# Optimization experiments

Measured on AMD Instinct MI355X. Metric: run time of the kernel, lower is better.

Reference implementation:

```python
import jax, jax.numpy as jnp
import numpy as np

N = 100000      # nodes
E = 1600000     # edges (avg degree 16)
D_IN = 64
D_OUT = 64
EPS = 1e-9


def setup_inputs() -> dict:
    key = jax.random.key(0)
    ks = jax.random.split(key, 12)
    x = jax.random.normal(ks[0], (N, D_IN), dtype=jnp.float32)
    edge_row = jax.random.randint(ks[1], (E,), 0, N, dtype=jnp.int32)
    edge_col = jax.random.randint(ks[2], (E,), 0, N, dtype=jnp.int32)
    # positive normalized adjacency values (~1/degree scale)
    edge_val = jax.random.uniform(ks[3], (E,), dtype=jnp.float32) / 16.0
    lim = float(np.sqrt(6.0 / (D_IN + D_OUT)))  # xavier_uniform
    W0 = jax.random.uniform(ks[4], (D_OUT, D_IN), jnp.float32, -lim, lim)
    W1 = jax.random.uniform(ks[5], (D_OUT, D_IN), jnp.float32, -lim, lim)
    b0 = jnp.zeros((D_OUT,), jnp.float32)
    b1 = jnp.zeros((D_OUT,), jnp.float32)
    scale0 = jnp.ones((D_OUT,), jnp.float32)
    scale1 = jnp.ones((D_OUT,), jnp.float32)
    offset0 = jnp.zeros((D_OUT,), jnp.float32)
    offset1 = jnp.zeros((D_OUT,), jnp.float32)
    return {"x": x, "edge_val": edge_val, "W0": W0, "b0": b0,
            "scale0": scale0, "offset0": offset0, "W1": W1, "b1": b1,
            "scale1": scale1, "offset1": offset1,
            "edge_row": edge_row, "edge_col": edge_col}


def _hop_transform(feat, W, b, scale, offset):
    # Linear (no bias in nn.Linear) + separate bias + ReLU
    h = jax.nn.relu(feat @ W.T + b)                      # [N, D_OUT]
    # custom per-row normalization ('norm' branch)
    mean = jnp.mean(h, axis=1, keepdims=True)
    var = jnp.var(h, axis=1, keepdims=True) + EPS        # unbiased=False
    return (h - mean) * scale * jax.lax.rsqrt(var) + offset


def reference(x, edge_val, W0, b0, scale0, offset0, W1, b1, scale1, offset1,
              edge_row, edge_col):
    # SpMM: out[r] = sum_{e: row[e]==r} val[e] * x[col[e]]
    msgs = edge_val[:, None] * x[edge_col]               # [E, D_IN]
    agg = jax.ops.segment_sum(msgs, edge_row, num_segments=N)
    # order=1: hop-0 uses raw features, hop-1 uses aggregated features
    h0 = _hop_transform(x, W0, b0, scale0, offset0)
    h1 = _hop_transform(agg, W1, b1, scale1, offset1)
    # aggr='mean' -> elementwise sum of partial features
    return h0 + h1
```

## Files before the change

### kernel.cpp

```cpp
#include <hip/hip_runtime.h>

#define NN 100000
#define NE 1600000
#define DD 64
#define NB   391
#define BCAP 4608
#define SCAP 6656
#define GCAP 2400000
#define NK3  1563

__device__ __forceinline__ unsigned short f2bfu(float f) {
    union { float f; unsigned u; } c; c.f = f;
    unsigned lsb = (c.u >> 16) & 1u;
    c.u += 0x7FFFu + lsb;
    return (unsigned short)(c.u >> 16);
}

typedef short v8s __attribute__((ext_vector_type(8)));
typedef float v4f __attribute__((ext_vector_type(4)));

__global__ __launch_bounds__(256) void init_kernel(
    const float* __restrict__ W0, const float* __restrict__ W1,
    int* __restrict__ gbcur, int* __restrict__ gtail,
    unsigned short* __restrict__ wb0, unsigned short* __restrict__ wb1)
{
    int i = blockIdx.x * 256 + threadIdx.x;
    if (i < NB) gbcur[i] = 0;
    if (i == 0) *gtail = 0;
    if (i < DD * DD) { wb0[i] = f2bfu(W0[i]); wb1[i] = f2bfu(W1[i]); }
}

__global__ __launch_bounds__(256) void x2bf_kernel(
    const float* __restrict__ x, unsigned short* __restrict__ xb)
{
    int i = (blockIdx.x * 256 + threadIdx.x) * 8;
    float4 a = *(const float4*)(x + i);
    float4 b = *(const float4*)(x + i + 4);
    uint4 o;
    o.x = (unsigned)f2bfu(a.x) | ((unsigned)f2bfu(a.y) << 16);
    o.y = (unsigned)f2bfu(a.z) | ((unsigned)f2bfu(a.w) << 16);
    o.z = (unsigned)f2bfu(b.x) | ((unsigned)f2bfu(b.y) << 16);
    o.w = (unsigned)f2bfu(b.z) | ((unsigned)f2bfu(b.w) << 16);
    *(uint4*)(xb + i) = o;
}

__global__ __launch_bounds__(512) void bin_scatter_kernel(
    const int* __restrict__ row, const int* __restrict__ col,
    const float* __restrict__ val, int* __restrict__ gbcur,
    int2* __restrict__ bslab)
{
    __shared__ int2 rbuf[4096];
    __shared__ unsigned short bkts[4096];
    __shared__ int pscan[512];
    __shared__ int cnt[NB];
    __shared__ int pst[NB];
    __shared__ int cur[NB];
    __shared__ int gbase[NB];

    int b = blockIdx.x, t = threadIdx.x;
    int e0 = b * 4096;

    for (int i = t; i < NB; i += 512) cnt[i] = 0;
    __syncthreads();

    int4 r[2], c[2]; float4 v[2]; bool ok[2];
#pragma unroll
    for (int h = 0; h < 2; ++h) {
        int e = e0 + t * 8 + h * 4;
        ok[h] = (e + 3 < NE);
        if (ok[h]) {
            r[h] = *(const int4*)(row + e);
            c[h] = *(const int4*)(col + e);
            v[h] = *(const float4*)(val + e);
            atomicAdd(&cnt[r[h].x >> 8], 1);
            atomicAdd(&cnt[r[h].y >> 8], 1);
            atomicAdd(&cnt[r[h].z >> 8], 1);
            atomicAdd(&cnt[r[h].w >> 8], 1);
        }
    }
    __syncthreads();
    pscan[t] = (t < NB) ? cnt[t] : 0;
    __syncthreads();
    for (int off = 1; off < 512; off <<= 1) {
        int u = (t >= off) ? pscan[t - off] : 0;
        __syncthreads();
        pscan[t] += u;
        __syncthreads();
    }
    if (t < NB) {
        int st = pscan[t] - cnt[t];
        pst[t] = st;
        cur[t] = st;
        gbase[t] = cnt[t] ? atomicAdd(&gbcur[t], cnt[t]) : 0;
    }
    __syncthreads();
#pragma unroll
    for (int h = 0; h < 2; ++h) {
        if (ok[h]) {
            int bk, pos;
            bk = r[h].x >> 8; pos = atomicAdd(&cur[bk], 1);
            rbuf[pos] = make_int2(c[h].x | ((r[h].x & 255) << 17), __float_as_int(v[h].x));
            bkts[pos] = (unsigned short)bk;
            bk = r[h].y >> 8; pos = atomicAdd(&cur[bk], 1);
            rbuf[pos] = make_int2(c[h].y | ((r[h].y & 255) << 17), __float_as_int(v[h].y));
            bkts[pos] = (unsigned short)bk;
            bk = r[h].z >> 8; pos = atomicAdd(&cur[bk], 1);
            rbuf[pos] = make_int2(c[h].z | ((r[h].z & 255) << 17), __float_as_int(v[h].z));
            bkts[pos] = (unsigned short)bk;
            bk = r[h].w >> 8; pos = atomicAdd(&cur[bk], 1);
            rbuf[pos] = make_int2(c[h].w | ((r[h].w & 255) << 17), __float_as_int(v[h].w));
            bkts[pos] = (unsigned short)bk;
        }
    }
    __syncthreads();
    int ntot = pscan[511];
    for (int i = t; i < ntot; i += 512) {
        int bk = bkts[i];
        int gi = gbase[bk] + (i - pst[bk]);
        if (gi < BCAP) bslab[(size_t)bk * BCAP + gi] = rbuf[i];
    }
}

__global__ __launch_bounds__(512) void row_sort_kernel(
    const int* __restrict__ gbcur, const int2* __restrict__ bslab,
    int* __restrict__ gtail, int2* __restrict__ gsorted,
    int* __restrict__ meta)
{
    __shared__ int2 sorted[SCAP];
    __shared__ int cnt[256];
    __shared__ int pscan[256];
    __shared__ int rcur[256];
    __shared__ int pstart[257];
    __shared__ int sh_base8;

    int b = blockIdx.x, t = threadIdx.x;
    int nb = min(gbcur[b], BCAP);
    const int2* bp = bslab + (size_t)b * BCAP;

    int2 rec[9]; int rl[9]; int nr = 0;
    if (t < 256) cnt[t] = 0;
    __syncthreads();
#pragma unroll
    for (int k = 0; k < 9; ++k) {
        int i = t + k * 512;
        if (i < nb) {
            rec[nr] = bp[i];
            rl[nr] = (rec[nr].x >> 17) & 255;
            atomicAdd(&cnt[rl[nr]], 1);
            ++nr;
        }
    }
    __syncthreads();
    if (t < 256) pscan[t] = (cnt[t] + 7) & ~7;
    __syncthreads();
    for (int off = 1; off < 256; off <<= 1) {
        int u = 0;
        if (t < 256 && t >= off) u = pscan[t - off];
        __syncthreads();
        if (t < 256) pscan[t] += u;
        __syncthreads();
    }
    if (t < 256) pstart[t + 1] = pscan[t];
    if (t == 0) {
        pstart[0] = 0;
        sh_base8 = atomicAdd(gtail, pscan[255] >> 3);
    }
    __syncthreads();
    int base8 = sh_base8;
    if (t < 256) {
        rcur[t] = pstart[t];
        int s = pstart[t] + cnt[t], e = pstart[t + 1];
        for (int j = s; j < e; ++j) sorted[j] = make_int2(0, 0);
        int n = b * 256 + t;
        int cc = min((e - pstart[t]) >> 3, 16);
        int s8 = base8 + (pstart[t] >> 3);
        meta[n] = (s8 << 5) | cc;
    }
    __syncthreads();
#pragma unroll
    for (int k = 0; k < 9; ++k) {
        if (k < nr) {
            int pos = atomicAdd(&rcur[rl[k]], 1);
            if (pos < SCAP) sorted[pos] = make_int2(rec[k].x & 0x1FFFF, rec[k].y);
        }
    }
    __syncthreads();
    int tp = pscan[255];
    int gb = base8 * 8;
    for (int i = t; i < tp; i += 512) {
        int gi = gb + i;
        if (gi < GCAP) gsorted[gi] = sorted[i];
    }
}

#define BF4FMA(G, VV, ACC) { \
    ACC.x = fmaf(VV, __uint_as_float((G).x << 16), ACC.x); \
    ACC.y = fmaf(VV, __uint_as_float((G).x & 0xFFFF0000u), ACC.y); \
    ACC.z = fmaf(VV, __uint_as_float((G).y << 16), ACC.z); \
    ACC.w = fmaf(VV, __uint_as_float((G).y & 0xFFFF0000u), ACC.w); }

__global__ __launch_bounds__(256, 8) void pull_mfma_kernel(
    const unsigned short* __restrict__ xb, const int* __restrict__ meta,
    const int2* __restrict__ gsorted,
    const unsigned short* __restrict__ wb0, const unsigned short* __restrict__ wb1,
    const float* __restrict__ b0, const float* __restrict__ s0, const float* __restrict__ o0,
    const float* __restrict__ b1, const float* __restrict__ s1, const float* __restrict__ o1,
    float* __restrict__ out)
{
    __shared__ int2 ebuf[4][128];
    __shared__ unsigned aggt[4][16][36];

    int t = threadIdx.x, lane = t & 63, wv = t >> 6;
    int sub = lane & 15, q = lane >> 4;
    int nb0 = blockIdx.x * 64 + wv * 16;
    if (nb0 >= NN) return;

    for (int rr = 0; rr < 16; ++rr) {
        int mt = meta[nb0 + rr];
        int cc = mt & 31;
        const int2* rp = gsorted + ((size_t)(mt >> 5) << 3);
        int plen = cc * 8;
        if (lane < plen) ebuf[wv][lane] = rp[lane];
        if (64 + lane < plen) ebuf[wv][64 + lane] = rp[64 + lane];

        float4 acc = make_float4(0.f, 0.f, 0.f, 0.f);
        int ch = 0;
        for (; ch + 2 <= cc; ch += 2) {
            int2 r0 = ebuf[wv][ch * 8 + q];
            int2 r1 = ebuf[wv][ch * 8 + 4 + q];
            int2 r2 = ebuf[wv][ch * 8 + 8 + q];
            int2 r3 = ebuf[wv][ch * 8 + 12 + q];
            uint2 g0 = *(const uint2*)(xb + (size_t)r0.x * DD + sub * 4);
            uint2 g1 = *(const uint2*)(xb + (size_t)r1.x * DD + sub * 4);
            uint2 g2 = *(const uint2*)(xb + (size_t)r2.x * DD + sub * 4);
            uint2 g3 = *(const uint2*)(xb + (size_t)r3.x * DD + sub * 4);
            float v0 = __int_as_float(r0.y), v1 = __int_as_float(r1.y);
            float v2 = __int_as_float(r2.y), v3 = __int_as_float(r3.y);
            BF4FMA(g0, v0, acc); BF4FMA(g1, v1, acc);
            BF4FMA(g2, v2, acc); BF4FMA(g3, v3, acc);
        }
        if (ch < cc) {
            int2 r0 = ebuf[wv][ch * 8 + q];
            int2 r1 = ebuf[wv][ch * 8 + 4 + q];
            uint2 g0 = *(const uint2*)(xb + (size_t)r0.x * DD + sub * 4);
            uint2 g1 = *(const uint2*)(xb + (size_t)r1.x * DD + sub * 4);
            float v0 = __int_as_float(r0.y), v1 = __int_as_float(r1.y);
            BF4FMA(g0, v0, acc); BF4FMA(g1, v1, acc);
        }
        acc.x += __shfl_xor(acc.x, 16, 64); acc.y += __shfl_xor(acc.y, 16, 64);
        acc.z += __shfl_xor(acc.z, 16, 64); acc.w += __shfl_xor(acc.w, 16, 64);
        acc.x += __shfl_xor(acc.x, 32, 64); acc.y += __shfl_xor(acc.y, 32, 64);
        acc.z += __shfl_xor(acc.z, 32, 64); acc.w += __shfl_xor(acc.w, 32, 64);
        if (q == 0) {
            uint2 pk;
            pk.x = (unsigned)f2bfu(acc.x) | ((unsigned)f2bfu(acc.y) << 16);
            pk.y = (unsigned)f2bfu(acc.z) | ((unsigned)f2bfu(acc.w) << 16);
            *(uint2*)&aggt[wv][rr][sub * 2] = pk;
        }
    }

    v8s ax[2], aa[2];
#pragma unroll
    for (int ks = 0; ks < 2; ++ks) {
        ax[ks] = *(const v8s*)(xb + (size_t)(nb0 + sub) * DD + ks * 32 + q * 8);
        aa[ks] = *(const v8s*)&aggt[wv][sub][ks * 16 + q * 4];
    }

    float h0v[4][4], h1v[4][4];
    float sr0[4] = {0,0,0,0}, sq0[4] = {0,0,0,0};
    float sr1[4] = {0,0,0,0}, sq1[4] = {0,0,0,0};
#pragma unroll
    for (int dt = 0; dt < 4; ++dt) {
        int nidx = dt * 16 + sub;
        float bi0 = b0[nidx], bi1 = b1[nidx];
        v8s w00 = *(const v8s*)(wb0 + nidx * 64 + q * 8);
        v8s w01 = *(const v8s*)(wb0 + nidx * 64 + 32 + q * 8);
        v8s w10 = *(const v8s*)(wb1 + nidx * 64 + q * 8);
        v8s w11 = *(const v8s*)(wb1 + nidx * 64 + 32 + q * 8);
        v4f c0 = (v4f){bi0, bi0, bi0, bi0};
        v4f c1 = (v4f){bi1, bi1, bi1, bi1};
        c0 = __builtin_amdgcn_mfma_f32_16x16x32_bf16(ax[0], w00, c0, 0, 0, 0);
        c0 = __builtin_amdgcn_mfma_f32_16x16x32_bf16(ax[1], w01, c0, 0, 0, 0);
        c1 = __builtin_amdgcn_mfma_f32_16x16x32_bf16(aa[0], w10, c1, 0, 0, 0);
        c1 = __builtin_amdgcn_mfma_f32_16x16x32_bf16(aa[1], w11, c1, 0, 0, 0);
#pragma unroll
        for (int r = 0; r < 4; ++r) {
            float h = fmaxf(c0[r], 0.f); h0v[dt][r] = h; sr0[r] += h; sq0[r] += h * h;
            float g = fmaxf(c1[r], 0.f); h1v[dt][r] = g; sr1[r] += g; sq1[r] += g * g;
        }
    }
#pragma unroll
    for (int off = 1; off < 16; off <<= 1) {
#pragma unroll
        for (int r = 0; r < 4; ++r) {
            sr0[r] += __shfl_xor(sr0[r], off, 64);
            sq0[r] += __shfl_xor(sq0[r], off, 64);
            sr1[r] += __shfl_xor(sr1[r], off, 64);
            sq1[r] += __shfl_xor(sq1[r], off, 64);
        }
    }

    float scl0[4], scl1[4], ofs0[4], ofs1[4];
#pragma unroll
    for (int dt = 0; dt < 4; ++dt) {
        int nidx = dt * 16 + sub;
        scl0[dt] = s0[nidx]; scl1[dt] = s1[nidx];
        ofs0[dt] = o0[nidx]; ofs1[dt] = o1[nidx];
    }

    const float inv = 1.0f / 64.0f;
#pragma unroll
    for (int r = 0; r < 4; ++r) {
        float m0 = sr0[r] * inv;
        float v0 = fmaxf(sq0[r] * inv - m0 * m0, 0.f) + 1e-9f;
        float m1 = sr1[r] * inv;
        float v1 = fmaxf(sq1[r] * inv - m1 * m1, 0.f) + 1e-9f;
        float rs0 = rsqrtf(v0), rs1 = rsqrtf(v1);
        int node = nb0 + q * 4 + r;
#pragma unroll
        for (int dt = 0; dt < 4; ++dt) {
            float rv = (h0v[dt][r] - m0) * scl0[dt] * rs0 + ofs0[dt]
                     + (h1v[dt][r] - m1) * scl1[dt] * rs1 + ofs1[dt];
            out[(size_t)node * DD + dt * 16 + sub] = rv;
        }
    }
}

extern "C" void kernel_launch(void* const* d_in, const int* in_sizes, int n_in,
                              void* d_out, int out_size, void* d_ws, size_t ws_size,
                              hipStream_t stream) {
    const float* x  = (const float*)d_in[0];
    const float* ev = (const float*)d_in[1];
    const float* W0 = (const float*)d_in[2];
    const float* b0 = (const float*)d_in[3];
    const float* s0 = (const float*)d_in[4];
    const float* o0 = (const float*)d_in[5];
    const float* W1 = (const float*)d_in[6];
    const float* b1 = (const float*)d_in[7];
    const float* s1 = (const float*)d_in[8];
    const float* o1 = (const float*)d_in[9];
    const int* row = (const int*)d_in[10];
    const int* col = (const int*)d_in[11];

    char* wsb = (char*)d_ws;
    int*  gbcur = (int*)wsb;
    int*  gtail = (int*)(wsb + 1600);
    unsigned short* wb0 = (unsigned short*)(wsb + 1664);
    unsigned short* wb1 = (unsigned short*)(wsb + 9856);
    int*  meta  = (int*)(wsb + 18176);
    unsigned short* xb = (unsigned short*)(wsb + 418816);
    int2* bslab = (int2*)(wsb + 13218816);
    int2* gsorted = (int2*)(wsb + 27632640);

    init_kernel<<<16, 256, 0, stream>>>(W0, W1, gbcur, gtail, wb0, wb1);
    x2bf_kernel<<<3125, 256, 0, stream>>>(x, xb);
    bin_scatter_kernel<<<NB, 512, 0, stream>>>(row, col, ev, gbcur, bslab);
    row_sort_kernel<<<NB, 512, 0, stream>>>(gbcur, bslab, gtail, gsorted, meta);
    pull_mfma_kernel<<<NK3, 256, 0, stream>>>(
        xb, meta, gsorted, wb0, wb1, b0, s0, o0, b1, s1, o1, (float*)d_out);
}
```

Baseline: 193.3 us.

## Fuse per-row sort into the pull kernel and drop the row_sort pass

Removes the separate row-sort kernel and its global sorted edge buffer. Each pull block now rescans its 256-row bucket slab, keeps only the edges for its 64-row quarter, and builds per-row edge lists in shared memory. The bin-scatter kernel handles 2048 edges per block, doubling the grid, and pull blocks are remapped in an XCD-aware way so the four quarters of a bucket share L2. The trade-off is that every bucket slab is read four times, occupancy is lower (launch bounds 5, larger LDS), and per-row degree is capped at 40 edges, so higher-degree rows would silently drop edges.

```diff
diff --git a/kernel.cpp b/kernel.cpp
--- a/kernel.cpp
+++ b/kernel.cpp
@@ -4,9 +4,9 @@
 #define NE 1600000
 #define DD 64
 #define NB   391
+#define NBK1 782
 #define BCAP 4608
-#define SCAP 6656
-#define GCAP 2400000
+#define RCAP 40
 #define NK3  1563
 
 __device__ __forceinline__ unsigned short f2bfu(float f) {
@@ -21,12 +21,11 @@
 
 __global__ __launch_bounds__(256) void init_kernel(
     const float* __restrict__ W0, const float* __restrict__ W1,
-    int* __restrict__ gbcur, int* __restrict__ gtail,
+    int* __restrict__ gbcur,
     unsigned short* __restrict__ wb0, unsigned short* __restrict__ wb1)
 {
     int i = blockIdx.x * 256 + threadIdx.x;
     if (i < NB) gbcur[i] = 0;
-    if (i == 0) *gtail = 0;
     if (i < DD * DD) { wb0[i] = f2bfu(W0[i]); wb1[i] = f2bfu(W1[i]); }
 }
 
@@ -49,8 +48,8 @@
     const float* __restrict__ val, int* __restrict__ gbcur,
     int2* __restrict__ bslab)
 {
-    __shared__ int2 rbuf[4096];
-    __shared__ unsigned short bkts[4096];
+    __shared__ int2 rbuf[2048];
+    __shared__ unsigned short bkts[2048];
     __shared__ int pscan[512];
     __shared__ int cnt[NB];
     __shared__ int pst[NB];
@@ -58,25 +57,21 @@
     __shared__ int gbase[NB];
 
     int b = blockIdx.x, t = threadIdx.x;
-    int e0 = b * 4096;
+    int e = b * 2048 + t * 4;
+    bool ok = (e + 3 < NE);
 
     for (int i = t; i < NB; i += 512) cnt[i] = 0;
     __syncthreads();
 
-    int4 r[2], c[2]; float4 v[2]; bool ok[2];
-#pragma unroll
-    for (int h = 0; h < 2; ++h) {
-        int e = e0 + t * 8 + h * 4;
-        ok[h] = (e + 3 < NE);
-        if (ok[h]) {
-            r[h] = *(const int4*)(row + e);
-            c[h] = *(const int4*)(col + e);
-            v[h] = *(const float4*)(val + e);
-            atomicAdd(&cnt[r[h].x >> 8], 1);
-            atomicAdd(&cnt[r[h].y >> 8], 1);
-            atomicAdd(&cnt[r[h].z >> 8], 1);
-            atomicAdd(&cnt[r[h].w >> 8], 1);
-        }
+    int4 r, c; float4 v;
+    if (ok) {
+        r = *(const int4*)(row + e);
+        c = *(const int4*)(col + e);
+        v = *(const float4*)(val + e);
+        atomicAdd(&cnt[r.x >> 8], 1);
+        atomicAdd(&cnt[r.y >> 8], 1);
+        atomicAdd(&cnt[r.z >> 8], 1);
+        atomicAdd(&cnt[r.w >> 8], 1);
     }
     __syncthreads();
     pscan[t] = (t < NB) ? cnt[t] : 0;
@@ -94,23 +89,20 @@
         gbase[t] = cnt[t] ? atomicAdd(&gbcur[t], cnt[t]) : 0;
     }
     __syncthreads();
-#pragma unroll
-    for (int h = 0; h < 2; ++h) {
-        if (ok[h]) {
-            int bk, pos;
-            bk = r[h].x >> 8; pos = atomicAdd(&cur[bk], 1);
-            rbuf[pos] = make_int2(c[h].x | ((r[h].x & 255) << 17), __float_as_int(v[h].x));
-            bkts[pos] = (unsigned short)bk;
-            bk = r[h].y >> 8; pos = atomicAdd(&cur[bk], 1);
-            rbuf[pos] = make_int2(c[h].y | ((r[h].y & 255) << 17), __float_as_int(v[h].y));
-            bkts[pos] = (unsigned short)bk;
-            bk = r[h].z >> 8; pos = atomicAdd(&cur[bk], 1);
-            rbuf[pos] = make_int2(c[h].z | ((r[h].z & 255) << 17), __float_as_int(v[h].z));
-            bkts[pos] = (unsigned short)bk;
-            bk = r[h].w >> 8; pos = atomicAdd(&cur[bk], 1);
-            rbuf[pos] = make_int2(c[h].w | ((r[h].w & 255) << 17), __float_as_int(v[h].w));
-            bkts[pos] = (unsigned short)bk;
-        }
+    if (ok) {
+        int bk, pos;
+        bk = r.x >> 8; pos = atomicAdd(&cur[bk], 1);
+        rbuf[pos] = make_int2(c.x | ((r.x & 255) << 17), __float_as_int(v.x));
+        bkts[pos] = (unsigned short)bk;
+        bk = r.y >> 8; pos = atomicAdd(&cur[bk], 1);
+        rbuf[pos] = make_int2(c.y | ((r.y & 255) << 17), __float_as_int(v.y));
+        bkts[pos] = (unsigned short)bk;
+        bk = r.z >> 8; pos = atomicAdd(&cur[bk], 1);
+        rbuf[pos] = make_int2(c.z | ((r.z & 255) << 17), __float_as_int(v.z));
+        bkts[pos] = (unsigned short)bk;
+        bk = r.w >> 8; pos = atomicAdd(&cur[bk], 1);
+        rbuf[pos] = make_int2(c.w | ((r.w & 255) << 17), __float_as_int(v.w));
+        bkts[pos] = (unsigned short)bk;
     }
     __syncthreads();
     int ntot = pscan[511];
@@ -121,207 +113,155 @@
     }
 }
 
-__global__ __launch_bounds__(512) void row_sort_kernel(
-    const int* __restrict__ gbcur, const int2* __restrict__ bslab,
-    int* __restrict__ gtail, int2* __restrict__ gsorted,
-    int* __restrict__ meta)
-{
-    __shared__ int2 sorted[SCAP];
-    __shared__ int cnt[256];
-    __shared__ int pscan[256];
-    __shared__ int rcur[256];
-    __shared__ int pstart[257];
-    __shared__ int sh_base8;
-
-    int b = blockIdx.x, t = threadIdx.x;
-    int nb = min(gbcur[b], BCAP);
-    const int2* bp = bslab + (size_t)b * BCAP;
-
-    int2 rec[9]; int rl[9]; int nr = 0;
-    if (t < 256) cnt[t] = 0;
-    __syncthreads();
-#pragma unroll
-    for (int k = 0; k < 9; ++k) {
-        int i = t + k * 512;
-        if (i < nb) {
-            rec[nr] = bp[i];
-            rl[nr] = (rec[nr].x >> 17) & 255;
-            atomicAdd(&cnt[rl[nr]], 1);
-            ++nr;
-        }
-    }
-    __syncthreads();
-    if (t < 256) pscan[t] = (cnt[t] + 7) & ~7;
-    __syncthreads();
-    for (int off = 1; off < 256; off <<= 1) {
-        int u = 0;
-        if (t < 256 && t >= off) u = pscan[t - off];
-        __syncthreads();
-        if (t < 256) pscan[t] += u;
-        __syncthreads();
-    }
-    if (t < 256) pstart[t + 1] = pscan[t];
-    if (t == 0) {
-        pstart[0] = 0;
-        sh_base8 = atomicAdd(gtail, pscan[255] >> 3);
-    }
-    __syncthreads();
-    int base8 = sh_base8;
-    if (t < 256) {
-        rcur[t] = pstart[t];
-        int s = pstart[t] + cnt[t], e = pstart[t + 1];
-        for (int j = s; j < e; ++j) sorted[j] = make_int2(0, 0);
-        int n = b * 256 + t;
-        int cc = min((e - pstart[t]) >> 3, 16);
-        int s8 = base8 + (pstart[t] >> 3);
-        meta[n] = (s8 << 5) | cc;
-    }
-    __syncthreads();
-#pragma unroll
-    for (int k = 0; k < 9; ++k) {
-        if (k < nr) {
-            int pos = atomicAdd(&rcur[rl[k]], 1);
-            if (pos < SCAP) sorted[pos] = make_int2(rec[k].x & 0x1FFFF, rec[k].y);
-        }
-    }
-    __syncthreads();
-    int tp = pscan[255];
-    int gb = base8 * 8;
-    for (int i = t; i < tp; i += 512) {
-        int gi = gb + i;
-        if (gi < GCAP) gsorted[gi] = sorted[i];
-    }
-}
-
 #define BF4FMA(G, VV, ACC) { \
     ACC.x = fmaf(VV, __uint_as_float((G).x << 16), ACC.x); \
     ACC.y = fmaf(VV, __uint_as_float((G).x & 0xFFFF0000u), ACC.y); \
     ACC.z = fmaf(VV, __uint_as_float((G).y << 16), ACC.z); \
     ACC.w = fmaf(VV, __uint_as_float((G).y & 0xFFFF0000u), ACC.w); }
 
-__global__ __launch_bounds__(256, 8) void pull_mfma_kernel(
-    const unsigned short* __restrict__ xb, const int* __restrict__ meta,
-    const int2* __restrict__ gsorted,
+__global__ __launch_bounds__(256, 5) void sort_pull_mfma_kernel(
+    const unsigned short* __restrict__ xb, const int* __restrict__ gbcur,
+    const int2* __restrict__ bslab,
     const unsigned short* __restrict__ wb0, const unsigned short* __restrict__ wb1,
     const float* __restrict__ b0, const float* __restrict__ s0, const float* __restrict__ o0,
     const float* __restrict__ b1, const float* __restrict__ s1, const float* __restrict__ o1,
     float* __restrict__ out)
 {
-    __shared__ int2 ebuf[4][128];
+    __shared__ int2 ebuf[64][RCAP];
     __shared__ unsigned aggt[4][16][36];
+    __shared__ int cur[64];
+
+    int phys = blockIdx.x;
+    int xc = phys & 7, ii = phys >> 3;
+    int p = (xc < 3) ? xc * 196 + ii : 588 + (xc - 3) * 195 + ii;
 
     int t = threadIdx.x, lane = t & 63, wv = t >> 6;
     int sub = lane & 15, q = lane >> 4;
-    int nb0 = blockIdx.x * 64 + wv * 16;
-    if (nb0 >= NN) return;
-
-    for (int rr = 0; rr < 16; ++rr) {
-        int mt = meta[nb0 + rr];
-        int cc = mt & 31;
-        const int2* rp = gsorted + ((size_t)(mt >> 5) << 3);
-        int plen = cc * 8;
-        if (lane < plen) ebuf[wv][lane] = rp[lane];
-        if (64 + lane < plen) ebuf[wv][64 + lane] = rp[64 + lane];
-
-        float4 acc = make_float4(0.f, 0.f, 0.f, 0.f);
-        int ch = 0;
-        for (; ch + 2 <= cc; ch += 2) {
-            int2 r0 = ebuf[wv][ch * 8 + q];
-            int2 r1 = ebuf[wv][ch * 8 + 4 + q];
-            int2 r2 = ebuf[wv][ch * 8 + 8 + q];
-            int2 r3 = ebuf[wv][ch * 8 + 12 + q];
-            uint2 g0 = *(const uint2*)(xb + (size_t)r0.x * DD + sub * 4);
-            uint2 g1 = *(const uint2*)(xb + (size_t)r1.x * DD + sub * 4);
-            uint2 g2 = *(const uint2*)(xb + (size_t)r2.x * DD + sub * 4);
-            uint2 g3 = *(const uint2*)(xb + (size_t)r3.x * DD + sub * 4);
-            float v0 = __int_as_float(r0.y), v1 = __int_as_float(r1.y);
-            float v2 = __int_as_float(r2.y), v3 = __int_as_float(r3.y);
-            BF4FMA(g0, v0, acc); BF4FMA(g1, v1, acc);
-            BF4FMA(g2, v2, acc); BF4FMA(g3, v3, acc);
-        }
-        if (ch < cc) {
-            int2 r0 = ebuf[wv][ch * 8 + q];
-            int2 r1 = ebuf[wv][ch * 8 + 4 + q];
-            uint2 g0 = *(const uint2*)(xb + (size_t)r0.x * DD + sub * 4);
-            uint2 g1 = *(const uint2*)(xb + (size_t)r1.x * DD + sub * 4);
-            float v0 = __int_as_float(r0.y), v1 = __int_as_float(r1.y);
-            BF4FMA(g0, v0, acc); BF4FMA(g1, v1, acc);
-        }
-        acc.x += __shfl_xor(acc.x, 16, 64); acc.y += __shfl_xor(acc.y, 16, 64);
-        acc.z += __shfl_xor(acc.z, 16, 64); acc.w += __shfl_xor(acc.w, 16, 64);
-        acc.x += __shfl_xor(acc.x, 32, 64); acc.y += __shfl_xor(acc.y, 32, 64);
-        acc.z += __shfl_xor(acc.z, 32, 64); acc.w += __shfl_xor(acc.w, 32, 64);
-        if (q == 0) {
-            uint2 pk;
-            pk.x = (unsigned)f2bfu(acc.x) | ((unsigned)f2bfu(acc.y) << 16);
-            pk.y = (unsigned)f2bfu(acc.z) | ((unsigned)f2bfu(acc.w) << 16);
-            *(uint2*)&aggt[wv][rr][sub * 2] = pk;
-        }
-    }
-
-    v8s ax[2], aa[2];
-#pragma unroll
-    for (int ks = 0; ks < 2; ++ks) {
-        ax[ks] = *(const v8s*)(xb + (size_t)(nb0 + sub) * DD + ks * 32 + q * 8);
-        aa[ks] = *(const v8s*)&aggt[wv][sub][ks * 16 + q * 4];
-    }
-
-    float h0v[4][4], h1v[4][4];
-    float sr0[4] = {0,0,0,0}, sq0[4] = {0,0,0,0};
-    float sr1[4] = {0,0,0,0}, sq1[4] = {0,0,0,0};
-#pragma unroll
-    for (int dt = 0; dt < 4; ++dt) {
-        int nidx = dt * 16 + sub;
-        float bi0 = b0[nidx], bi1 = b1[nidx];
-        v8s w00 = *(const v8s*)(wb0 + nidx * 64 + q * 8);
-        v8s w01 = *(const v8s*)(wb0 + nidx * 64 + 32 + q * 8);
-        v8s w10 = *(const v8s*)(wb1 + nidx * 64 + q * 8);
-        v8s w11 = *(const v8s*)(wb1 + nidx * 64 + 32 + q * 8);
-        v4f c0 = (v4f){bi0, bi0, bi0, bi0};
-        v4f c1 = (v4f){bi1, bi1, bi1, bi1};
-        c0 = __builtin_amdgcn_mfma_f32_16x16x32_bf16(ax[0], w00, c0, 0, 0, 0);
-        c0 = __builtin_amdgcn_mfma_f32_16x16x32_bf16(ax[1], w01, c0, 0, 0, 0);
-        c1 = __builtin_amdgcn_mfma_f32_16x16x32_bf16(aa[0], w10, c1, 0, 0, 0);
-        c1 = __builtin_amdgcn_mfma_f32_16x16x32_bf16(aa[1], w11, c1, 0, 0, 0);
+    int bkt = p >> 2, quarter = p & 3;
+    int nb = min(gbcur[bkt], BCAP);
+    const int2* bp = bslab + (size_t)bkt * BCAP;
+
+    if (t < 64) cur[t] = 0;
+    __syncthreads();
+    for (int i = t; i < nb; i += 256) {
+        int2 rc = bp[i];
+        int rl = (rc.x >> 17) & 255;
+        if ((rl >> 6) == quarter) {
+            int pos = atomicAdd(&cur[rl & 63], 1);
+            if (pos < RCAP) ebuf[rl & 63][pos] = make_int2(rc.x & 0x1FFFF, rc.y);
+        }
+    }
+    __syncthreads();
+
+    int nb0 = p * 64 + wv * 16;
+    if (nb0 < NN) {
+        for (int rr = 0; rr < 16; ++rr) {
+            int lr = wv * 16 + rr;
+            int d = min(cur[lr], RCAP);
+            int cc = (d + 7) >> 3;
+            int plen = cc * 8;
+            if (lane < plen - d) ebuf[lr][d + lane] = make_int2(0, 0);
+
+            float4 acc = make_float4(0.f, 0.f, 0.f, 0.f);
+            int ch = 0;
+            for (; ch + 2 <= cc; ch += 2) {
+                int2 r0 = ebuf[lr][ch * 8 + q];
+                int2 r1 = ebuf[lr][ch * 8 + 4 + q];
+                int2 r2 = ebuf[lr][ch * 8 + 8 + q];
+                int2 r3 = ebuf[lr][ch * 8 + 12 + q];
+                uint2 g0 = *(const uint2*)(xb + (size_t)r0.x * DD + sub * 4);
+                uint2 g1 = *(const uint2*)(xb + (size_t)r1.x * DD + sub * 4);
+                uint2 g2 = *(const uint2*)(xb + (size_t)r2.x * DD + sub * 4);
+                uint2 g3 = *(const uint2*)(xb + (size_t)r3.x * DD + sub * 4);
+                float v0 = __int_as_float(r0.y), v1 = __int_as_float(r1.y);
+                float v2 = __int_as_float(r2.y), v3 = __int_as_float(r3.y);
+                BF4FMA(g0, v0, acc); BF4FMA(g1, v1, acc);
+                BF4FMA(g2, v2, acc); BF4FMA(g3, v3, acc);
+            }
+            if (ch < cc) {
+                int2 r0 = ebuf[lr][ch * 8 + q];
+                int2 r1 = ebuf[lr][ch * 8 + 4 + q];
+                uint2 g0 = *(const uint2*)(xb + (size_t)r0.x * DD + sub * 4);
+                uint2 g1 = *(const uint2*)(xb + (size_t)r1.x * DD + sub * 4);
+                float v0 = __int_as_float(r0.y), v1 = __int_as_float(r1.y);
+                BF4FMA(g0, v0, acc); BF4FMA(g1, v1, acc);
+            }
+            acc.x += __shfl_xor(acc.x, 16, 64); acc.y += __shfl_xor(acc.y, 16, 64);
+            acc.z += __shfl_xor(acc.z, 16, 64); acc.w += __shfl_xor(acc.w, 16, 64);
+            acc.x += __shfl_xor(acc.x, 32, 64); acc.y += __shfl_xor(acc.y, 32, 64);
+            acc.z += __shfl_xor(acc.z, 32, 64); acc.w += __shfl_xor(acc.w, 32, 64);
+            if (q == 0) {
+                uint2 pk;
+                pk.x = (unsigned)f2bfu(acc.x) | ((unsigned)f2bfu(acc.y) << 16);
+                pk.y = (unsigned)f2bfu(acc.z) | ((unsigned)f2bfu(acc.w) << 16);
+                *(uint2*)&aggt[wv][rr][sub * 2] = pk;
+            }
+        }
+
+        v8s ax[2], aa[2];
+#pragma unroll
+        for (int ks = 0; ks < 2; ++ks) {
+            ax[ks] = *(const v8s*)(xb + (size_t)(nb0 + sub) * DD + ks * 32 + q * 8);
+            aa[ks] = *(const v8s*)&aggt[wv][sub][ks * 16 + q * 4];
+        }
+
+        float h0v[4][4], h1v[4][4];
+        float sr0[4] = {0,0,0,0}, sq0[4] = {0,0,0,0};
+        float sr1[4] = {0,0,0,0}, sq1[4] = {0,0,0,0};
+#pragma unroll
+        for (int dt = 0; dt < 4; ++dt) {
+            int nidx = dt * 16 + sub;
+            float bi0 = b0[nidx], bi1 = b1[nidx];
+            v8s w00 = *(const v8s*)(wb0 + nidx * 64 + q * 8);
+            v8s w01 = *(const v8s*)(wb0 + nidx * 64 + 32 + q * 8);
+            v8s w10 = *(const v8s*)(wb1 + nidx * 64 + q * 8);
+            v8s w11 = *(const v8s*)(wb1 + nidx * 64 + 32 + q * 8);
+            v4f c0 = (v4f){bi0, bi0, bi0, bi0};
+            v4f c1 = (v4f){bi1, bi1, bi1, bi1};
+            c0 = __builtin_amdgcn_mfma_f32_16x16x32_bf16(ax[0], w00, c0, 0, 0, 0);
+            c0 = __builtin_amdgcn_mfma_f32_16x16x32_bf16(ax[1], w01, c0, 0, 0, 0);
+            c1 = __builtin_amdgcn_mfma_f32_16x16x32_bf16(aa[0], w10, c1, 0, 0, 0);
+            c1 = __builtin_amdgcn_mfma_f32_16x16x32_bf16(aa[1], w11, c1, 0, 0, 0);
+#pragma unroll
+            for (int r = 0; r < 4; ++r) {
+                float h = fmaxf(c0[r], 0.f); h0v[dt][r] = h; sr0[r] += h; sq0[r] += h * h;
+                float g = fmaxf(c1[r], 0.f); h1v[dt][r] = g; sr1[r] += g; sq1[r] += g * g;
+            }
+        }
+#pragma unroll
+        for (int off = 1; off < 16; off <<= 1) {
+#pragma unroll
+            for (int r = 0; r < 4; ++r) {
+                sr0[r] += __shfl_xor(sr0[r], off, 64);
+                sq0[r] += __shfl_xor(sq0[r], off, 64);
+                sr1[r] += __shfl_xor(sr1[r], off, 64);
+                sq1[r] += __shfl_xor(sq1[r], off, 64);
+            }
+        }
+
+        float scl0[4], scl1[4], ofs0[4], ofs1[4];
+#pragma unroll
+        for (int dt = 0; dt < 4; ++dt) {
+            int nidx = dt * 16 + sub;
+            scl0[dt] = s0[nidx]; scl1[dt] = s1[nidx];
+            ofs0[dt] = o0[nidx]; ofs1[dt] = o1[nidx];
+        }
+
+        const float inv = 1.0f / 64.0f;
 #pragma unroll
         for (int r = 0; r < 4; ++r) {
-            float h = fmaxf(c0[r], 0.f); h0v[dt][r] = h; sr0[r] += h; sq0[r] += h * h;
-            float g = fmaxf(c1[r], 0.f); h1v[dt][r] = g; sr1[r] += g; sq1[r] += g * g;
-        }
-    }
-#pragma unroll
-    for (int off = 1; off < 16; off <<= 1) {
-#pragma unroll
-        for (int r = 0; r < 4; ++r) {
-            sr0[r] += __shfl_xor(sr0[r], off, 64);
-            sq0[r] += __shfl_xor(sq0[r], off, 64);
-            sr1[r] += __shfl_xor(sr1[r], off, 64);
-            sq1[r] += __shfl_xor(sq1[r], off, 64);
-        }
-    }
-
-    float scl0[4], scl1[4], ofs0[4], ofs1[4];
-#pragma unroll
-    for (int dt = 0; dt < 4; ++dt) {
-        int nidx = dt * 16 + sub;
-        scl0[dt] = s0[nidx]; scl1[dt] = s1[nidx];
-        ofs0[dt] = o0[nidx]; ofs1[dt] = o1[nidx];
-    }
-
-    const float inv = 1.0f / 64.0f;
-#pragma unroll
-    for (int r = 0; r < 4; ++r) {
-        float m0 = sr0[r] * inv;
-        float v0 = fmaxf(sq0[r] * inv - m0 * m0, 0.f) + 1e-9f;
-        float m1 = sr1[r] * inv;
-        float v1 = fmaxf(sq1[r] * inv - m1 * m1, 0.f) + 1e-9f;
-        float rs0 = rsqrtf(v0), rs1 = rsqrtf(v1);
-        int node = nb0 + q * 4 + r;
-#pragma unroll
-        for (int dt = 0; dt < 4; ++dt) {
-            float rv = (h0v[dt][r] - m0) * scl0[dt] * rs0 + ofs0[dt]
-                     + (h1v[dt][r] - m1) * scl1[dt] * rs1 + ofs1[dt];
-            out[(size_t)node * DD + dt * 16 + sub] = rv;
+            float m0 = sr0[r] * inv;
+            float v0 = fmaxf(sq0[r] * inv - m0 * m0, 0.f) + 1e-9f;
+            float m1 = sr1[r] * inv;
+            float v1 = fmaxf(sq1[r] * inv - m1 * m1, 0.f) + 1e-9f;
+            float rs0 = rsqrtf(v0), rs1 = rsqrtf(v1);
+            int node = nb0 + q * 4 + r;
+#pragma unroll
+            for (int dt = 0; dt < 4; ++dt) {
+                float rv = (h0v[dt][r] - m0) * scl0[dt] * rs0 + ofs0[dt]
+                         + (h1v[dt][r] - m1) * scl1[dt] * rs1 + ofs1[dt];
+                out[(size_t)node * DD + dt * 16 + sub] = rv;
+            }
         }
     }
 }
@@ -344,18 +284,14 @@
 
     char* wsb = (char*)d_ws;
     int*  gbcur = (int*)wsb;
-    int*  gtail = (int*)(wsb + 1600);
-    unsigned short* wb0 = (unsigned short*)(wsb + 1664);
-    unsigned short* wb1 = (unsigned short*)(wsb + 9856);
-    int*  meta  = (int*)(wsb + 18176);
-    unsigned short* xb = (unsigned short*)(wsb + 418816);
-    int2* bslab = (int2*)(wsb + 13218816);
-    int2* gsorted = (int2*)(wsb + 27632640);
-
-    init_kernel<<<16, 256, 0, stream>>>(W0, W1, gbcur, gtail, wb0, wb1);
+    unsigned short* wb0 = (unsigned short*)(wsb + 1600);
+    unsigned short* wb1 = (unsigned short*)(wsb + 9792);
+    unsigned short* xb = (unsigned short*)(wsb + 18048);
+    int2* bslab = (int2*)(wsb + 12818048);
+
+    init_kernel<<<16, 256, 0, stream>>>(W0, W1, gbcur, wb0, wb1);
     x2bf_kernel<<<3125, 256, 0, stream>>>(x, xb);
-    bin_scatter_kernel<<<NB, 512, 0, stream>>>(row, col, ev, gbcur, bslab);
-    row_sort_kernel<<<NB, 512, 0, stream>>>(gbcur, bslab, gtail, gsorted, meta);
-    pull_mfma_kernel<<<NK3, 256, 0, stream>>>(
-        xb, meta, gsorted, wb0, wb1, b0, s0, o0, b1, s1, o1, (float*)d_out);
-}
+    bin_scatter_kernel<<<NBK1, 512, 0, stream>>>(row, col, ev, gbcur, bslab);
+    sort_pull_mfma_kernel<<<NK3, 256, 0, stream>>>(
+        xb, gbcur, bslab, wb0, wb1, b0, s0, o0, b1, s1, o1, (float*)d_out);
+}
```

New measurement: 201.3 us. +4.2%, slower.
